# Performance work log

Measured on AMD Instinct MI355X. Metric: run time of the kernel, lower is better.

## Reference

```python
import jax, jax.numpy as jnp
import numpy as np

B, S, D, H, R = 4, 1024, 1024, 16, 4
HD = D // H
EPS = 1e-5


def layer_norm(x, g, b):
    mu = jnp.mean(x, axis=-1, keepdims=True)
    var = jnp.mean(jnp.square(x - mu), axis=-1, keepdims=True)
    return (x - mu) * jax.lax.rsqrt(var + EPS) * g + b


def setup_inputs() -> dict:
    key = jax.random.key(0)
    ks = jax.random.split(key, 12)
    sd = 1.0 / np.sqrt(D)
    sf = 1.0 / np.sqrt(R * D)
    inp = {
        "x": jax.random.normal(ks[0], (B, S, D), jnp.float32),
        "ln1_g": jnp.ones((D,), jnp.float32),
        "ln1_b": jnp.zeros((D,), jnp.float32),
        "wq": jax.random.uniform(ks[1], (D, D), jnp.float32, -sd, sd),
        "bq": jnp.zeros((D,), jnp.float32),
        "wk": jax.random.uniform(ks[2], (D, D), jnp.float32, -sd, sd),
        "bk": jnp.zeros((D,), jnp.float32),
        "wv": jax.random.uniform(ks[3], (D, D), jnp.float32, -sd, sd),
        "bv": jnp.zeros((D,), jnp.float32),
        "wo": jax.random.uniform(ks[4], (D, D), jnp.float32, -sd, sd),
        "bo": jnp.zeros((D,), jnp.float32),
        "ln2_g": jnp.ones((D,), jnp.float32),
        "ln2_b": jnp.zeros((D,), jnp.float32),
        "w1": jax.random.uniform(ks[5], (D, R * D), jnp.float32, -sd, sd),
        "b1": jnp.zeros((R * D,), jnp.float32),
        "w2": jax.random.uniform(ks[6], (R * D, D), jnp.float32, -sf, sf),
        "b2": jnp.zeros((D,), jnp.float32),
    }
    return inp


def reference(x, ln1_g, ln1_b, wq, bq, wk, bk, wv, bv, wo, bo,
              ln2_g, ln2_b, w1, b1, w2, b2):
    # Pre-LN MHA. Per-head Q/K/V linears concatenated == one batched projection
    # reshaped into heads, so we batch all heads in single GEMMs.
    h = layer_norm(x, ln1_g, ln1_b)
    q = (h @ wq + bq).reshape(B, S, H, HD)
    k = (h @ wk + bk).reshape(B, S, H, HD)
    v = (h @ wv + bv).reshape(B, S, H, HD)
    scores = jnp.einsum("bqhd,bkhd->bhqk", q, k) / np.sqrt(HD)
    attn = jax.nn.softmax(scores, axis=-1)
    ctx = jnp.einsum("bhqk,bkhd->bqhd", attn, v).reshape(B, S, D)
    x = x + ctx @ wo + bo
    # Pre-LN MLP with exact (erf) GELU, matching torch nn.GELU default.
    h2 = layer_norm(x, ln2_g, ln2_b)
    mlp = jax.nn.gelu(h2 @ w1 + b1, approximate=False) @ w2 + b2
    return x + mlp
```

## Files before the change

### kernel.cpp

```cpp
#include <hip/hip_runtime.h>

typedef unsigned short u16;
typedef __attribute__((ext_vector_type(8))) __bf16 bf16x8;
typedef __attribute__((ext_vector_type(4))) float floatx4;

#define FLAG_F32OUT  1
#define FLAG_GELU    2
#define FLAG_PARTIAL 4
#define FLAG_PBF16   8

__device__ __forceinline__ u16 f2bf(float f) {
  union { float f; unsigned u; } un;
  un.f = f;
  unsigned u = un.u;
  u += 0x7fffu + ((u >> 16) & 1u);
  return (u16)(u >> 16);
}

__device__ __forceinline__ float bf2f(u16 h) {
  union { unsigned u; float f; } un;
  un.u = ((unsigned)h) << 16;
  return un.f;
}

__device__ __forceinline__ float gelu_f(float x) {
  float t = 1.5957691216f * (x + 0.044715f * x * x * x);
  return x / (1.0f + __expf(-t));
}

__device__ __forceinline__ floatx4 mfma16(bf16x8 a, bf16x8 b, floatx4 c) {
  return __builtin_amdgcn_mfma_f32_16x16x32_bf16(a, b, c, 0, 0, 0);
}

__device__ __forceinline__ void glds16(const void* g, void* l) {
  __builtin_amdgcn_global_load_lds(
      (__attribute__((address_space(1))) unsigned int*)(void*)g,
      (__attribute__((address_space(3))) unsigned int*)l, 16, 0, 0);
}

__global__ __launch_bounds__(256) void prep_all(
    const float* __restrict__ wq, const float* __restrict__ wk,
    const float* __restrict__ wv, const float* __restrict__ wo,
    const float* __restrict__ w1, const float* __restrict__ w2,
    const float* __restrict__ bq, const float* __restrict__ bk,
    const float* __restrict__ bv,
    u16* __restrict__ wqkvt, u16* __restrict__ wot,
    u16* __restrict__ w1t, u16* __restrict__ w2t,
    float* __restrict__ bqkv) {
  int b = blockIdx.x;
  int tx = threadIdx.x, ty = threadIdx.y;
  if (b >= 12288) {
    int i = (b - 12288) * 256 + ty * 32 + tx;
    float v = (i < 1024) ? bq[i] * 0.125f
                         : (i < 2048 ? bk[i - 1024] : bv[i - 2048]);
    bqkv[i] = v;
    return;
  }
  const float* W;
  u16* Wt;
  int K, N, bx, by;
  float scale = 1.0f;
  if (b < 4096) {
    int w = b >> 10, t = b & 1023;
    bx = t & 31; by = t >> 5; K = 1024; N = 1024;
    if (w == 0)      { W = wq; Wt = wqkvt;                scale = 0.125f; }
    else if (w == 1) { W = wk; Wt = wqkvt + 1024 * 1024; }
    else if (w == 2) { W = wv; Wt = wqkvt + 2 * 1024 * 1024; }
    else             { W = wo; Wt = wot; }
  } else if (b < 8192) {
    int t = b - 4096;
    bx = t & 127; by = t >> 7; K = 1024; N = 4096; W = w1; Wt = w1t;
  } else {
    int t = b - 8192;
    bx = t & 31; by = t >> 5; K = 4096; N = 1024; W = w2; Wt = w2t;
  }
  __shared__ float tile[32][33];
  int n0 = bx * 32, k0 = by * 32;
#pragma unroll
  for (int i = 0; i < 4; ++i)
    tile[ty + i * 8][tx] = W[(size_t)(k0 + ty + i * 8) * N + n0 + tx];
  __syncthreads();
#pragma unroll
  for (int i = 0; i < 4; ++i)
    Wt[(size_t)(n0 + ty + i * 8) * K + k0 + tx] =
        f2bf(tile[tx][ty + i * 8] * scale);
}

__global__ __launch_bounds__(256) void ln_kernel(
    const float* __restrict__ x, const float* __restrict__ g,
    const float* __restrict__ b, u16* __restrict__ out) {
  int row = blockIdx.x;
  int tid = threadIdx.x;
  const float4* xr = (const float4*)(x + (size_t)row * 1024);
  float4 v = xr[tid];
  float s = v.x + v.y + v.z + v.w;
  float s2 = v.x * v.x + v.y * v.y + v.z * v.z + v.w * v.w;
#pragma unroll
  for (int m = 32; m >= 1; m >>= 1) {
    s += __shfl_xor(s, m, 64);
    s2 += __shfl_xor(s2, m, 64);
  }
  __shared__ float red[8];
  int wave = tid >> 6, lane = tid & 63;
  if (lane == 0) { red[wave] = s; red[4 + wave] = s2; }
  __syncthreads();
  s = red[0] + red[1] + red[2] + red[3];
  s2 = red[4] + red[5] + red[6] + red[7];
  float mu = s * (1.0f / 1024.0f);
  float var = s2 * (1.0f / 1024.0f) - mu * mu;
  float inv = rsqrtf(var + 1e-5f);
  float4 gv = ((const float4*)g)[tid];
  float4 bv = ((const float4*)b)[tid];
  ushort4 ov;
  ov.x = f2bf((v.x - mu) * inv * gv.x + bv.x);
  ov.y = f2bf((v.y - mu) * inv * gv.y + bv.y);
  ov.z = f2bf((v.z - mu) * inv * gv.z + bv.z);
  ov.w = f2bf((v.w - mu) * inv * gv.w + bv.w);
  *(ushort4*)(out + (size_t)row * 1024 + tid * 4) = ov;
}

__global__ __launch_bounds__(256, 4) void gemm_bt(
    const u16* __restrict__ A, const u16* __restrict__ Bt,
    const float* __restrict__ bias,
    void* __restrict__ outp, void* __restrict__ outp2,
    int M, int N, int K, int Ks, int flags) {
  __shared__ __align__(16) u16 smem[17408];
  u16* As = smem;
  u16* Bs = smem + 8192;
  int tid = threadIdx.x;
  int lane = tid & 63, wave = tid >> 6;
  int lm = lane & 15, quad = lane >> 4;
  int wm = (wave >> 1) * 64, wn = (wave & 1) * 64;
  int bm = blockIdx.x, bn = blockIdx.y;
  int koff = blockIdx.z * Ks;

  const u16* aP = A + (size_t)(bm * 128 + (tid >> 2)) * K + koff + (tid & 3) * 8;
  const u16* bP = Bt + (size_t)(bn * 128 + (tid >> 2)) * K + koff + (tid & 3) * 8;
  u16* asD = As + tid * 8;
  u16* bsD = Bs + tid * 8;
  size_t rstep = (size_t)64 * K;

  floatx4 acc[4][4];
#pragma unroll
  for (int i = 0; i < 4; ++i)
#pragma unroll
    for (int j = 0; j < 4; ++j) acc[i][j] = (floatx4){0.f, 0.f, 0.f, 0.f};

  for (int k0 = 0; k0 < Ks; k0 += 64) {
#pragma unroll
    for (int p = 0; p < 2; ++p) {
      glds16(aP + p * 32, asD + p * 4096);
      glds16(aP + p * 32 + rstep, asD + p * 4096 + 2048);
      glds16(bP + p * 32, bsD + p * 4096);
      glds16(bP + p * 32 + rstep, bsD + p * 4096 + 2048);
    }
    aP += 64;
    bP += 64;
    __syncthreads();
#pragma unroll
    for (int p = 0; p < 2; ++p) {
      bf16x8 af[4], bfr[4];
#pragma unroll
      for (int mi = 0; mi < 4; ++mi)
        af[mi] = *(const bf16x8*)&As[p * 4096 + (wm + mi * 16 + lm) * 32 + quad * 8];
#pragma unroll
      for (int ni = 0; ni < 4; ++ni)
        bfr[ni] = *(const bf16x8*)&Bs[p * 4096 + (wn + ni * 16 + lm) * 32 + quad * 8];
#pragma unroll
      for (int mi = 0; mi < 4; ++mi)
#pragma unroll
        for (int ni = 0; ni < 4; ++ni)
          acc[mi][ni] = mfma16(af[mi], bfr[ni], acc[mi][ni]);
    }
    __syncthreads();
  }

  bool gelu = (flags & FLAG_GELU) != 0;
  bool part = (flags & FLAG_PARTIAL) != 0;
  bool pbf = (flags & FLAG_PBF16) != 0;
  bool f32p = ((flags & FLAG_F32OUT) != 0) ||
              (part && !(pbf && blockIdx.z > 0));
  void* op;
  if (blockIdx.z == 0)
    op = outp;
  else
    op = (char*)outp2 +
         (size_t)(blockIdx.z - 1) * M * N * (pbf ? 2 : 4);

  if (!f32p) {
    u16* Ct = smem;
#pragma unroll
    for (int ni = 0; ni < 4; ++ni) {
      int col = bn * 128 + wn + ni * 16 + lm;
      float bv = part ? 0.0f : bias[col];
#pragma unroll
      for (int mi = 0; mi < 4; ++mi) {
        int lr0 = wm + mi * 16 + quad * 4;
#pragma unroll
        for (int r = 0; r < 4; ++r) {
          float vv = acc[mi][ni][r] + bv;
          if (gelu) vv = gelu_f(vv);
          Ct[(lr0 + r) * 136 + wn + ni * 16 + lm] = f2bf(vv);
        }
      }
    }
    __syncthreads();
#pragma unroll
    for (int p = 0; p < 8; ++p) {
      int unit = p * 256 + tid;
      int row = unit >> 4, ch = unit & 15;
      uint4 v = *(const uint4*)&Ct[row * 136 + ch * 8];
      *(uint4*)&((u16*)op)[(size_t)(bm * 128 + row) * N + bn * 128 + ch * 8] = v;
    }
  } else {
    float* Cf = (float*)smem;
#pragma unroll
    for (int pp = 0; pp < 2; ++pp) {
      __syncthreads();
      if ((wave >> 1) == pp) {
#pragma unroll
        for (int ni = 0; ni < 4; ++ni) {
          int col = bn * 128 + wn + ni * 16 + lm;
          float bv = part ? 0.0f : bias[col];
#pragma unroll
          for (int mi = 0; mi < 4; ++mi) {
            int lr0 = mi * 16 + quad * 4;
#pragma unroll
            for (int r = 0; r < 4; ++r) {
              float vv = acc[mi][ni][r] + bv;
              if (gelu) vv = gelu_f(vv);
              Cf[(lr0 + r) * 132 + wn + ni * 16 + lm] = vv;
            }
          }
        }
      }
      __syncthreads();
#pragma unroll
      for (int p = 0; p < 8; ++p) {
        int unit = p * 256 + tid;
        int row = unit >> 5, ch = unit & 31;
        float4 v = *(const float4*)&Cf[row * 132 + ch * 4];
        size_t gi = (size_t)(bm * 128 + pp * 64 + row) * N + bn * 128 + ch * 4;
        *(float4*)&((float*)op)[gi] = v;
      }
    }
  }
}

__global__ __launch_bounds__(512) void flash_attn(
    const u16* __restrict__ qkv, u16* __restrict__ ctx) {
  __shared__ __align__(16) u16 Qs[128 * 72];
  __shared__ __align__(16) u16 Ks[64 * 72];
  __shared__ __align__(16) u16 Vt[64 * 64];

  int tid = threadIdx.x;
  int lane = tid & 63, wave = tid >> 6;
  int lm = lane & 15, quad = lane >> 4;
  int qt = blockIdx.x & 7;
  int hh = (blockIdx.x >> 3) & 15;
  int b = blockIdx.x >> 7;

  int krow = tid >> 3;
  int col8 = (tid & 7) * 8;
  int cb = col8 >> 3;

  size_t base_q = ((size_t)(b * 1024 + qt * 128)) * 3072 + hh * 64;
#pragma unroll
  for (int r = 0; r < 2; ++r) {
    int idx = r * 512 + tid;
    int row = idx >> 3;
    int c8 = (idx & 7) * 8;
    *(uint4*)&Qs[row * 72 + c8] =
        *(const uint4*)&qkv[base_q + (size_t)row * 3072 + c8];
  }
  __syncthreads();
  bf16x8 a0 = *(const bf16x8*)&Qs[(wave * 16 + lm) * 72 + quad * 8];
  bf16x8 a1 = *(const bf16x8*)&Qs[(wave * 16 + lm) * 72 + 32 + quad * 8];
  u16* Ps = &Qs[wave * 16 * 72];

  float l_r[4];
  floatx4 acc[4];
#pragma unroll
  for (int r = 0; r < 4; ++r) l_r[r] = 0.0f;
#pragma unroll
  for (int d = 0; d < 4; ++d) acc[d] = (floatx4){0.f, 0.f, 0.f, 0.f};

  size_t kv0 = ((size_t)(b * 1024 + krow)) * 3072 + 1024 + hh * 64 + col8;
  const size_t kv_step = (size_t)64 * 3072;

  uint4 kreg = *(const uint4*)&qkv[kv0];
  uint4 vreg = *(const uint4*)&qkv[kv0 + 1024];

  int rw = krow >> 3;
  int rl = krow & 7;

  for (int j = 0; j < 16; ++j) {
    __syncthreads();
    *(uint4*)&Ks[krow * 72 + col8] = kreg;
    {
      u16* ve = (u16*)&vreg;
#pragma unroll
      for (int e = 0; e < 8; ++e) {
        int d = col8 + e;
        int chunk = (rw ^ cb ^ e) & 7;
        Vt[d * 64 + chunk * 8 + rl] = ve[e];
      }
    }
    __syncthreads();

    if (j < 15) {
      size_t kvn = kv0 + (size_t)(j + 1) * kv_step;
      kreg = *(const uint4*)&qkv[kvn];
      vreg = *(const uint4*)&qkv[kvn + 1024];
    }

    floatx4 sacc[4];
#pragma unroll
    for (int ni = 0; ni < 4; ++ni) {
      bf16x8 b0 = *(const bf16x8*)&Ks[(ni * 16 + lm) * 72 + quad * 8];
      bf16x8 b1 = *(const bf16x8*)&Ks[(ni * 16 + lm) * 72 + 32 + quad * 8];
      floatx4 z = (floatx4){0.f, 0.f, 0.f, 0.f};
      z = mfma16(a0, b0, z);
      z = mfma16(a1, b1, z);
      sacc[ni] = z;
    }

#pragma unroll
    for (int r = 0; r < 4; ++r) {
      float p0 = __expf(sacc[0][r]);
      float p1 = __expf(sacc[1][r]);
      float p2 = __expf(sacc[2][r]);
      float p3 = __expf(sacc[3][r]);
      l_r[r] += (p0 + p1) + (p2 + p3);
      Ps[(quad * 4 + r) * 72 + 0 * 16 + lm] = f2bf(p0);
      Ps[(quad * 4 + r) * 72 + 1 * 16 + lm] = f2bf(p1);
      Ps[(quad * 4 + r) * 72 + 2 * 16 + lm] = f2bf(p2);
      Ps[(quad * 4 + r) * 72 + 3 * 16 + lm] = f2bf(p3);
    }

    bf16x8 pa0 = *(const bf16x8*)&Ps[lm * 72 + quad * 8];
    bf16x8 pa1 = *(const bf16x8*)&Ps[lm * 72 + 32 + quad * 8];
#pragma unroll
    for (int dd = 0; dd < 4; ++dd) {
      int d = dd * 16 + lm;
      int dx = ((d >> 3) ^ d) & 7;
      bf16x8 vb0 = *(const bf16x8*)&Vt[d * 64 + ((quad ^ dx) & 7) * 8];
      bf16x8 vb1 = *(const bf16x8*)&Vt[d * 64 + (((4 + quad) ^ dx) & 7) * 8];
      acc[dd] = mfma16(pa0, vb0, acc[dd]);
      acc[dd] = mfma16(pa1, vb1, acc[dd]);
    }
  }

  float rl4[4];
#pragma unroll
  for (int r = 0; r < 4; ++r) {
    float sm = l_r[r];
#pragma unroll
    for (int mm = 1; mm < 16; mm <<= 1) sm += __shfl_xor(sm, mm, 64);
    rl4[r] = 1.0f / sm;
  }
#pragma unroll
  for (int dd = 0; dd < 4; ++dd)
#pragma unroll
    for (int r = 0; r < 4; ++r)
      Ps[(quad * 4 + r) * 72 + dd * 16 + lm] = f2bf(acc[dd][r] * rl4[r]);
  size_t obase = (size_t)(b * 1024 + qt * 128 + wave * 16);
#pragma unroll
  for (int p = 0; p < 2; ++p) {
    int unit = p * 64 + lane;
    int row = unit >> 3, ch = unit & 7;
    uint4 v = *(const uint4*)&Ps[row * 72 + ch * 8];
    *(uint4*)&ctx[(obase + row) * 1024 + hh * 64 + ch * 8] = v;
  }
}

__global__ __launch_bounds__(256) void reduce_ln(
    float* __restrict__ x2, const float* __restrict__ p1,
    const float* __restrict__ x, const float* __restrict__ bo,
    const float* __restrict__ g, const float* __restrict__ bb,
    u16* __restrict__ h2) {
  int row = blockIdx.x, tid = threadIdx.x;
  size_t base = (size_t)row * 256;
  float4 a = ((const float4*)x2)[base + tid];
  float4 p = ((const float4*)p1)[base + tid];
  float4 c = ((const float4*)x)[base + tid];
  float4 d = ((const float4*)bo)[tid];
  float4 o;
  o.x = a.x + p.x + c.x + d.x;
  o.y = a.y + p.y + c.y + d.y;
  o.z = a.z + p.z + c.z + d.z;
  o.w = a.w + p.w + c.w + d.w;
  ((float4*)x2)[base + tid] = o;

  float s = o.x + o.y + o.z + o.w;
  float s2 = o.x * o.x + o.y * o.y + o.z * o.z + o.w * o.w;
#pragma unroll
  for (int m = 32; m >= 1; m >>= 1) {
    s += __shfl_xor(s, m, 64);
    s2 += __shfl_xor(s2, m, 64);
  }
  __shared__ float red[8];
  int wave = tid >> 6, lane = tid & 63;
  if (lane == 0) { red[wave] = s; red[4 + wave] = s2; }
  __syncthreads();
  s = red[0] + red[1] + red[2] + red[3];
  s2 = red[4] + red[5] + red[6] + red[7];
  float mu = s * (1.0f / 1024.0f);
  float var = s2 * (1.0f / 1024.0f) - mu * mu;
  float inv = rsqrtf(var + 1e-5f);
  float4 gv = ((const float4*)g)[tid];
  float4 bv = ((const float4*)bb)[tid];
  ushort4 ov;
  ov.x = f2bf((o.x - mu) * inv * gv.x + bv.x);
  ov.y = f2bf((o.y - mu) * inv * gv.y + bv.y);
  ov.z = f2bf((o.z - mu) * inv * gv.z + bv.z);
  ov.w = f2bf((o.w - mu) * inv * gv.w + bv.w);
  *(ushort4*)(h2 + (size_t)row * 1024 + tid * 4) = ov;
}

__global__ __launch_bounds__(256) void reduce4b(
    float* __restrict__ out, const u16* __restrict__ pb,
    const float* __restrict__ resid, const float* __restrict__ bias) {
  int i = blockIdx.x * 256 + threadIdx.x;
  float4 a = ((const float4*)out)[i];
  ushort4 q0 = ((const ushort4*)pb)[i];
  ushort4 q1 = ((const ushort4*)(pb + 4194304))[i];
  ushort4 q2 = ((const ushort4*)(pb + 8388608))[i];
  float4 c = ((const float4*)resid)[i];
  float4 d = ((const float4*)bias)[i & 255];
  float4 o;
  o.x = a.x + bf2f(q0.x) + bf2f(q1.x) + bf2f(q2.x) + c.x + d.x;
  o.y = a.y + bf2f(q0.y) + bf2f(q1.y) + bf2f(q2.y) + c.y + d.y;
  o.z = a.z + bf2f(q0.z) + bf2f(q1.z) + bf2f(q2.z) + c.z + d.z;
  o.w = a.w + bf2f(q0.w) + bf2f(q1.w) + bf2f(q2.w) + c.w + d.w;
  ((float4*)out)[i] = o;
}

extern "C" void kernel_launch(void* const* d_in, const int* in_sizes, int n_in,
                              void* d_out, int out_size, void* d_ws, size_t ws_size,
                              hipStream_t stream) {
  const float* x    = (const float*)d_in[0];
  const float* ln1g = (const float*)d_in[1];
  const float* ln1b = (const float*)d_in[2];
  const float* wq   = (const float*)d_in[3];
  const float* bq   = (const float*)d_in[4];
  const float* wk   = (const float*)d_in[5];
  const float* bk   = (const float*)d_in[6];
  const float* wv   = (const float*)d_in[7];
  const float* bv   = (const float*)d_in[8];
  const float* wo   = (const float*)d_in[9];
  const float* bo   = (const float*)d_in[10];
  const float* ln2g = (const float*)d_in[11];
  const float* ln2b = (const float*)d_in[12];
  const float* w1   = (const float*)d_in[13];
  const float* b1   = (const float*)d_in[14];
  const float* w2   = (const float*)d_in[15];
  const float* b2   = (const float*)d_in[16];

  char* ws = (char*)d_ws;
  const size_t MB = 1024ull * 1024ull;
  u16*   h     = (u16*)(ws + 0 * MB);
  u16*   h2    = (u16*)(ws + 0 * MB);
  u16*   qkv   = (u16*)(ws + 8 * MB);
  float* pwo   = (float*)(ws + 8 * MB);
  u16*   act   = (u16*)(ws + 8 * MB);
  u16*   ctxb  = (u16*)(ws + 32 * MB);
  float* bqkv  = (float*)(ws + 32 * MB);
  float* x2    = (float*)(ws + 40 * MB);
  u16*   pw2   = (u16*)(ws + 56 * MB);
  u16*   wqkvt = (u16*)(ws + 64 * MB);
  u16*   wot   = (u16*)(ws + 70 * MB);
  u16*   w1t   = (u16*)(ws + 72 * MB);
  u16*   w2t   = (u16*)(ws + 80 * MB);

  prep_all<<<12300, dim3(32, 8), 0, stream>>>(
      wq, wk, wv, wo, w1, w2, bq, bk, bv, wqkvt, wot, w1t, w2t, bqkv);

  ln_kernel<<<4096, 256, 0, stream>>>(x, ln1g, ln1b, h);

  gemm_bt<<<dim3(32, 24, 1), 256, 0, stream>>>(
      h, wqkvt, bqkv, (void*)qkv, nullptr, 4096, 3072, 1024, 1024, 0);

  flash_attn<<<512, 512, 0, stream>>>(qkv, ctxb);

  gemm_bt<<<dim3(32, 8, 2), 256, 0, stream>>>(
      ctxb, wot, nullptr, (void*)x2, (void*)pwo, 4096, 1024, 1024, 512,
      FLAG_PARTIAL);
  reduce_ln<<<4096, 256, 0, stream>>>(x2, pwo, x, bo, ln2g, ln2b, h2);

  gemm_bt<<<dim3(32, 32, 1), 256, 0, stream>>>(
      h2, w1t, b1, (void*)act, nullptr, 4096, 4096, 1024, 1024, FLAG_GELU);

  gemm_bt<<<dim3(32, 8, 4), 256, 0, stream>>>(
      act, w2t, nullptr, d_out, (void*)pw2, 4096, 1024, 4096, 1024,
      FLAG_PARTIAL | FLAG_PBF16);
  reduce4b<<<4096, 256, 0, stream>>>((float*)d_out, pw2, x2, b2);
}
```

Before: 326.5 us.

## Double-buffer GEMM K-loop and fold first LayerNorm into weight-prep launch

The GEMM main loop now loads 32-wide K slices into two LDS halves, issuing the next slice's global-to-LDS copy before computing on the current one. This lets memory transfer overlap MFMA work instead of waiting behind a full barrier every 64 columns. Separately, the first LayerNorm runs as extra blocks appended to the weight-prep kernel, which removes one launch. The trade-offs are more barriers per iteration and an added sync before the epilogue's reuse of shared memory.

Measured after the change: 328.3 us. About the same (+0.6%).

```diff
diff --git a/kernel.cpp b/kernel.cpp
--- a/kernel.cpp
+++ b/kernel.cpp
@@ -46,11 +46,44 @@
     const float* __restrict__ bv,
     u16* __restrict__ wqkvt, u16* __restrict__ wot,
     u16* __restrict__ w1t, u16* __restrict__ w2t,
-    float* __restrict__ bqkv) {
+    float* __restrict__ bqkv,
+    const float* __restrict__ x, const float* __restrict__ ln1g,
+    const float* __restrict__ ln1b, u16* __restrict__ h) {
   int b = blockIdx.x;
   int tx = threadIdx.x, ty = threadIdx.y;
+  int tid = ty * 32 + tx;
+  if (b >= 12300) {
+    int row = b - 12300;
+    const float4* xr = (const float4*)(x + (size_t)row * 1024);
+    float4 v = xr[tid];
+    float s = v.x + v.y + v.z + v.w;
+    float s2 = v.x * v.x + v.y * v.y + v.z * v.z + v.w * v.w;
+#pragma unroll
+    for (int m = 32; m >= 1; m >>= 1) {
+      s += __shfl_xor(s, m, 64);
+      s2 += __shfl_xor(s2, m, 64);
+    }
+    __shared__ float red[8];
+    int wave = tid >> 6, lane = tid & 63;
+    if (lane == 0) { red[wave] = s; red[4 + wave] = s2; }
+    __syncthreads();
+    s = red[0] + red[1] + red[2] + red[3];
+    s2 = red[4] + red[5] + red[6] + red[7];
+    float mu = s * (1.0f / 1024.0f);
+    float var = s2 * (1.0f / 1024.0f) - mu * mu;
+    float inv = rsqrtf(var + 1e-5f);
+    float4 gv = ((const float4*)ln1g)[tid];
+    float4 bv2 = ((const float4*)ln1b)[tid];
+    ushort4 ov;
+    ov.x = f2bf((v.x - mu) * inv * gv.x + bv2.x);
+    ov.y = f2bf((v.y - mu) * inv * gv.y + bv2.y);
+    ov.z = f2bf((v.z - mu) * inv * gv.z + bv2.z);
+    ov.w = f2bf((v.w - mu) * inv * gv.w + bv2.w);
+    *(ushort4*)(h + (size_t)row * 1024 + tid * 4) = ov;
+    return;
+  }
   if (b >= 12288) {
-    int i = (b - 12288) * 256 + ty * 32 + tx;
+    int i = (b - 12288) * 256 + tid;
     float v = (i < 1024) ? bq[i] * 0.125f
                          : (i < 2048 ? bk[i - 1024] : bv[i - 2048]);
     bqkv[i] = v;
@@ -86,39 +119,6 @@
         f2bf(tile[tx][ty + i * 8] * scale);
 }
 
-__global__ __launch_bounds__(256) void ln_kernel(
-    const float* __restrict__ x, const float* __restrict__ g,
-    const float* __restrict__ b, u16* __restrict__ out) {
-  int row = blockIdx.x;
-  int tid = threadIdx.x;
-  const float4* xr = (const float4*)(x + (size_t)row * 1024);
-  float4 v = xr[tid];
-  float s = v.x + v.y + v.z + v.w;
-  float s2 = v.x * v.x + v.y * v.y + v.z * v.z + v.w * v.w;
-#pragma unroll
-  for (int m = 32; m >= 1; m >>= 1) {
-    s += __shfl_xor(s, m, 64);
-    s2 += __shfl_xor(s2, m, 64);
-  }
-  __shared__ float red[8];
-  int wave = tid >> 6, lane = tid & 63;
-  if (lane == 0) { red[wave] = s; red[4 + wave] = s2; }
-  __syncthreads();
-  s = red[0] + red[1] + red[2] + red[3];
-  s2 = red[4] + red[5] + red[6] + red[7];
-  float mu = s * (1.0f / 1024.0f);
-  float var = s2 * (1.0f / 1024.0f) - mu * mu;
-  float inv = rsqrtf(var + 1e-5f);
-  float4 gv = ((const float4*)g)[tid];
-  float4 bv = ((const float4*)b)[tid];
-  ushort4 ov;
-  ov.x = f2bf((v.x - mu) * inv * gv.x + bv.x);
-  ov.y = f2bf((v.y - mu) * inv * gv.y + bv.y);
-  ov.z = f2bf((v.z - mu) * inv * gv.z + bv.z);
-  ov.w = f2bf((v.w - mu) * inv * gv.w + bv.w);
-  *(ushort4*)(out + (size_t)row * 1024 + tid * 4) = ov;
-}
-
 __global__ __launch_bounds__(256, 4) void gemm_bt(
     const u16* __restrict__ A, const u16* __restrict__ Bt,
     const float* __restrict__ bias,
@@ -146,26 +146,30 @@
 #pragma unroll
     for (int j = 0; j < 4; ++j) acc[i][j] = (floatx4){0.f, 0.f, 0.f, 0.f};
 
-  for (int k0 = 0; k0 < Ks; k0 += 64) {
-#pragma unroll
-    for (int p = 0; p < 2; ++p) {
-      glds16(aP + p * 32, asD + p * 4096);
-      glds16(aP + p * 32 + rstep, asD + p * 4096 + 2048);
-      glds16(bP + p * 32, bsD + p * 4096);
-      glds16(bP + p * 32 + rstep, bsD + p * 4096 + 2048);
-    }
-    aP += 64;
-    bP += 64;
-    __syncthreads();
-#pragma unroll
-    for (int p = 0; p < 2; ++p) {
+  glds16(aP, asD);
+  glds16(aP + rstep, asD + 2048);
+  glds16(bP, bsD);
+  glds16(bP + rstep, bsD + 2048);
+  aP += 32;
+  bP += 32;
+
+  int nIter = Ks >> 5;
+  for (int it = 0; it < nIter; it += 2) {
+    __syncthreads();
+    glds16(aP, asD + 4096);
+    glds16(aP + rstep, asD + 4096 + 2048);
+    glds16(bP, bsD + 4096);
+    glds16(bP + rstep, bsD + 4096 + 2048);
+    aP += 32;
+    bP += 32;
+    {
       bf16x8 af[4], bfr[4];
 #pragma unroll
       for (int mi = 0; mi < 4; ++mi)
-        af[mi] = *(const bf16x8*)&As[p * 4096 + (wm + mi * 16 + lm) * 32 + quad * 8];
+        af[mi] = *(const bf16x8*)&As[(wm + mi * 16 + lm) * 32 + quad * 8];
 #pragma unroll
       for (int ni = 0; ni < 4; ++ni)
-        bfr[ni] = *(const bf16x8*)&Bs[p * 4096 + (wn + ni * 16 + lm) * 32 + quad * 8];
+        bfr[ni] = *(const bf16x8*)&Bs[(wn + ni * 16 + lm) * 32 + quad * 8];
 #pragma unroll
       for (int mi = 0; mi < 4; ++mi)
 #pragma unroll
@@ -173,6 +177,28 @@
           acc[mi][ni] = mfma16(af[mi], bfr[ni], acc[mi][ni]);
     }
     __syncthreads();
+    if (it + 2 < nIter) {
+      glds16(aP, asD);
+      glds16(aP + rstep, asD + 2048);
+      glds16(bP, bsD);
+      glds16(bP + rstep, bsD + 2048);
+      aP += 32;
+      bP += 32;
+    }
+    {
+      bf16x8 af[4], bfr[4];
+#pragma unroll
+      for (int mi = 0; mi < 4; ++mi)
+        af[mi] = *(const bf16x8*)&As[4096 + (wm + mi * 16 + lm) * 32 + quad * 8];
+#pragma unroll
+      for (int ni = 0; ni < 4; ++ni)
+        bfr[ni] = *(const bf16x8*)&Bs[4096 + (wn + ni * 16 + lm) * 32 + quad * 8];
+#pragma unroll
+      for (int mi = 0; mi < 4; ++mi)
+#pragma unroll
+        for (int ni = 0; ni < 4; ++ni)
+          acc[mi][ni] = mfma16(af[mi], bfr[ni], acc[mi][ni]);
+    }
   }
 
   bool gelu = (flags & FLAG_GELU) != 0;
@@ -189,6 +215,7 @@
 
   if (!f32p) {
     u16* Ct = smem;
+    __syncthreads();
 #pragma unroll
     for (int ni = 0; ni < 4; ++ni) {
       int col = bn * 128 + wn + ni * 16 + lm;
@@ -473,10 +500,9 @@
   u16*   w1t   = (u16*)(ws + 72 * MB);
   u16*   w2t   = (u16*)(ws + 80 * MB);
 
-  prep_all<<<12300, dim3(32, 8), 0, stream>>>(
-      wq, wk, wv, wo, w1, w2, bq, bk, bv, wqkvt, wot, w1t, w2t, bqkv);
-
-  ln_kernel<<<4096, 256, 0, stream>>>(x, ln1g, ln1b, h);
+  prep_all<<<16396, dim3(32, 8), 0, stream>>>(
+      wq, wk, wv, wo, w1, w2, bq, bk, bv, wqkvt, wot, w1t, w2t, bqkv,
+      x, ln1g, ln1b, h);
 
   gemm_bt<<<dim3(32, 24, 1), 256, 0, stream>>>(
       h, wqkvt, bqkv, (void*)qkv, nullptr, 4096, 3072, 1024, 1024, 0);
```

## Double-buffer K/V tiles in flash attention and fuse LN1 into prep kernel

Applied to the files above, without the earlier changes.

Flash attention now alternates between two shared-memory K/V buffers, removing one barrier per key tile so stores to the next tile can overlap compute on the previous one. The first layer norm moves into the weight-prep kernel as extra blocks, which removes a separate launch. In exchange, shared-memory use per attention block goes up and the prep kernel's grid grows.

Measured after the change: 328.1 us. Within noise of the previous version (+0.5%).

```diff
diff --git a/kernel.cpp b/kernel.cpp
--- a/kernel.cpp
+++ b/kernel.cpp
@@ -46,11 +46,44 @@
     const float* __restrict__ bv,
     u16* __restrict__ wqkvt, u16* __restrict__ wot,
     u16* __restrict__ w1t, u16* __restrict__ w2t,
-    float* __restrict__ bqkv) {
+    float* __restrict__ bqkv,
+    const float* __restrict__ x, const float* __restrict__ ln1g,
+    const float* __restrict__ ln1b, u16* __restrict__ h) {
   int b = blockIdx.x;
   int tx = threadIdx.x, ty = threadIdx.y;
+  int tid = ty * 32 + tx;
+  if (b >= 12300) {
+    int row = b - 12300;
+    const float4* xr = (const float4*)(x + (size_t)row * 1024);
+    float4 v = xr[tid];
+    float s = v.x + v.y + v.z + v.w;
+    float s2 = v.x * v.x + v.y * v.y + v.z * v.z + v.w * v.w;
+#pragma unroll
+    for (int m = 32; m >= 1; m >>= 1) {
+      s += __shfl_xor(s, m, 64);
+      s2 += __shfl_xor(s2, m, 64);
+    }
+    __shared__ float red[8];
+    int wave = tid >> 6, lane = tid & 63;
+    if (lane == 0) { red[wave] = s; red[4 + wave] = s2; }
+    __syncthreads();
+    s = red[0] + red[1] + red[2] + red[3];
+    s2 = red[4] + red[5] + red[6] + red[7];
+    float mu = s * (1.0f / 1024.0f);
+    float var = s2 * (1.0f / 1024.0f) - mu * mu;
+    float inv = rsqrtf(var + 1e-5f);
+    float4 gv = ((const float4*)ln1g)[tid];
+    float4 bv2 = ((const float4*)ln1b)[tid];
+    ushort4 ov;
+    ov.x = f2bf((v.x - mu) * inv * gv.x + bv2.x);
+    ov.y = f2bf((v.y - mu) * inv * gv.y + bv2.y);
+    ov.z = f2bf((v.z - mu) * inv * gv.z + bv2.z);
+    ov.w = f2bf((v.w - mu) * inv * gv.w + bv2.w);
+    *(ushort4*)(h + (size_t)row * 1024 + tid * 4) = ov;
+    return;
+  }
   if (b >= 12288) {
-    int i = (b - 12288) * 256 + ty * 32 + tx;
+    int i = (b - 12288) * 256 + tid;
     float v = (i < 1024) ? bq[i] * 0.125f
                          : (i < 2048 ? bk[i - 1024] : bv[i - 2048]);
     bqkv[i] = v;
@@ -86,39 +119,6 @@
         f2bf(tile[tx][ty + i * 8] * scale);
 }
 
-__global__ __launch_bounds__(256) void ln_kernel(
-    const float* __restrict__ x, const float* __restrict__ g,
-    const float* __restrict__ b, u16* __restrict__ out) {
-  int row = blockIdx.x;
-  int tid = threadIdx.x;
-  const float4* xr = (const float4*)(x + (size_t)row * 1024);
-  float4 v = xr[tid];
-  float s = v.x + v.y + v.z + v.w;
-  float s2 = v.x * v.x + v.y * v.y + v.z * v.z + v.w * v.w;
-#pragma unroll
-  for (int m = 32; m >= 1; m >>= 1) {
-    s += __shfl_xor(s, m, 64);
-    s2 += __shfl_xor(s2, m, 64);
-  }
-  __shared__ float red[8];
-  int wave = tid >> 6, lane = tid & 63;
-  if (lane == 0) { red[wave] = s; red[4 + wave] = s2; }
-  __syncthreads();
-  s = red[0] + red[1] + red[2] + red[3];
-  s2 = red[4] + red[5] + red[6] + red[7];
-  float mu = s * (1.0f / 1024.0f);
-  float var = s2 * (1.0f / 1024.0f) - mu * mu;
-  float inv = rsqrtf(var + 1e-5f);
-  float4 gv = ((const float4*)g)[tid];
-  float4 bv = ((const float4*)b)[tid];
-  ushort4 ov;
-  ov.x = f2bf((v.x - mu) * inv * gv.x + bv.x);
-  ov.y = f2bf((v.y - mu) * inv * gv.y + bv.y);
-  ov.z = f2bf((v.z - mu) * inv * gv.z + bv.z);
-  ov.w = f2bf((v.w - mu) * inv * gv.w + bv.w);
-  *(ushort4*)(out + (size_t)row * 1024 + tid * 4) = ov;
-}
-
 __global__ __launch_bounds__(256, 4) void gemm_bt(
     const u16* __restrict__ A, const u16* __restrict__ Bt,
     const float* __restrict__ bias,
@@ -250,8 +250,8 @@
 __global__ __launch_bounds__(512) void flash_attn(
     const u16* __restrict__ qkv, u16* __restrict__ ctx) {
   __shared__ __align__(16) u16 Qs[128 * 72];
-  __shared__ __align__(16) u16 Ks[64 * 72];
-  __shared__ __align__(16) u16 Vt[64 * 64];
+  __shared__ __align__(16) u16 Ks[2][64 * 72];
+  __shared__ __align__(16) u16 Vt[2][64 * 64];
 
   int tid = threadIdx.x;
   int lane = tid & 63, wave = tid >> 6;
@@ -295,30 +295,30 @@
   int rl = krow & 7;
 
   for (int j = 0; j < 16; ++j) {
-    __syncthreads();
-    *(uint4*)&Ks[krow * 72 + col8] = kreg;
+    u16* KsB = Ks[j & 1];
+    u16* VtB = Vt[j & 1];
+    *(uint4*)&KsB[krow * 72 + col8] = kreg;
     {
       u16* ve = (u16*)&vreg;
 #pragma unroll
       for (int e = 0; e < 8; ++e) {
         int d = col8 + e;
         int chunk = (rw ^ cb ^ e) & 7;
-        Vt[d * 64 + chunk * 8 + rl] = ve[e];
+        VtB[d * 64 + chunk * 8 + rl] = ve[e];
       }
     }
-    __syncthreads();
-
     if (j < 15) {
       size_t kvn = kv0 + (size_t)(j + 1) * kv_step;
       kreg = *(const uint4*)&qkv[kvn];
       vreg = *(const uint4*)&qkv[kvn + 1024];
     }
+    __syncthreads();
 
     floatx4 sacc[4];
 #pragma unroll
     for (int ni = 0; ni < 4; ++ni) {
-      bf16x8 b0 = *(const bf16x8*)&Ks[(ni * 16 + lm) * 72 + quad * 8];
-      bf16x8 b1 = *(const bf16x8*)&Ks[(ni * 16 + lm) * 72 + 32 + quad * 8];
+      bf16x8 b0 = *(const bf16x8*)&KsB[(ni * 16 + lm) * 72 + quad * 8];
+      bf16x8 b1 = *(const bf16x8*)&KsB[(ni * 16 + lm) * 72 + 32 + quad * 8];
       floatx4 z = (floatx4){0.f, 0.f, 0.f, 0.f};
       z = mfma16(a0, b0, z);
       z = mfma16(a1, b1, z);
@@ -344,8 +344,8 @@
     for (int dd = 0; dd < 4; ++dd) {
       int d = dd * 16 + lm;
       int dx = ((d >> 3) ^ d) & 7;
-      bf16x8 vb0 = *(const bf16x8*)&Vt[d * 64 + ((quad ^ dx) & 7) * 8];
-      bf16x8 vb1 = *(const bf16x8*)&Vt[d * 64 + (((4 + quad) ^ dx) & 7) * 8];
+      bf16x8 vb0 = *(const bf16x8*)&VtB[d * 64 + ((quad ^ dx) & 7) * 8];
+      bf16x8 vb1 = *(const bf16x8*)&VtB[d * 64 + (((4 + quad) ^ dx) & 7) * 8];
       acc[dd] = mfma16(pa0, vb0, acc[dd]);
       acc[dd] = mfma16(pa1, vb1, acc[dd]);
     }
@@ -473,10 +473,9 @@
   u16*   w1t   = (u16*)(ws + 72 * MB);
   u16*   w2t   = (u16*)(ws + 80 * MB);
 
-  prep_all<<<12300, dim3(32, 8), 0, stream>>>(
-      wq, wk, wv, wo, w1, w2, bq, bk, bv, wqkvt, wot, w1t, w2t, bqkv);
-
-  ln_kernel<<<4096, 256, 0, stream>>>(x, ln1g, ln1b, h);
+  prep_all<<<16396, dim3(32, 8), 0, stream>>>(
+      wq, wk, wv, wo, w1, w2, bq, bk, bv, wqkvt, wot, w1t, w2t, bqkv,
+      x, ln1g, ln1b, h);
 
   gemm_bt<<<dim3(32, 24, 1), 256, 0, stream>>>(
       h, wqkvt, bqkv, (void*)qkv, nullptr, 4096, 3072, 1024, 1024, 0);
```
